# Kernel optimization log

Measured on AMD Instinct MI355X. Metric: run time of the kernel, lower is better.

## Reference

```python
import jax, jax.numpy as jnp
import numpy as np

B, SQ, SK, E, H = 2, 256, 512, 512, 256

def _lin_init(k, fan_in, fan_out):
    return jax.random.normal(k, (fan_in, fan_out), jnp.float32) / np.sqrt(fan_in)

def setup_inputs() -> dict:
    key = jax.random.key(0)
    ks = jax.random.split(key, 16)
    inp = {
        'query': jax.random.normal(ks[0], (B, SQ, E), jnp.float32),
        'key':   jax.random.normal(ks[1], (B, SK, E), jnp.float32),
        # encoders
        'Wqe': _lin_init(ks[2], E, H), 'bqe': jnp.zeros((H,), jnp.float32),
        'Wke': _lin_init(ks[3], E, H), 'bke': jnp.zeros((H,), jnp.float32),
        # importance predictor: Linear(2H,H) x1, Linear(H,H) x2, Linear(H,1)
        'W0': _lin_init(ks[4], 2 * H, H), 'b0': jnp.zeros((H,), jnp.float32),
        'W1': _lin_init(ks[5], H, H),     'b1': jnp.zeros((H,), jnp.float32),
        'W2': _lin_init(ks[6], H, H),     'b2': jnp.zeros((H,), jnp.float32),
        'Wf': _lin_init(ks[7], H, 1),     'bf': jnp.zeros((1,), jnp.float32),
        # variance estimator: Linear(2H,H), Linear(H,1), Softplus
        'Wv1': _lin_init(ks[8], 2 * H, H), 'bv1': jnp.zeros((H,), jnp.float32),
        'Wv2': _lin_init(ks[9], H, 1),     'bv2': jnp.zeros((1,), jnp.float32),
    }
    return inp

def reference(query, key, Wqe, bqe, Wke, bke, W0, b0, W1, b1, W2, b2, Wf, bf, Wv1, bv1, Wv2, bv2):
    # Encoders (dropout is identity at eval): [B,Sq,H] and [B,Sk,H]
    qf = jax.nn.relu(jnp.einsum('bqe,eh->bqh', query, Wqe) + bqe)
    kf = jax.nn.relu(jnp.einsum('bke,eh->bkh', key, Wke) + bke)

    # concat([qf, kf]) @ W == qf @ W[:H] + kf @ W[H:]; avoid materializing the 2H concat
    Hd = qf.shape[-1]
    # importance predictor, layer 0 over all (q,k) pairs -> [B,Sq,Sk,H]
    q_part = jnp.einsum('bqh,hd->bqd', qf, W0[:Hd])
    k_part = jnp.einsum('bkh,hd->bkd', kf, W0[Hd:])
    h = jax.nn.relu(q_part[:, :, None, :] + k_part[:, None, :, :] + b0)
    h = jax.nn.relu(jnp.einsum('bqkh,hd->bqkd', h, W1) + b1)
    h = jax.nn.relu(jnp.einsum('bqkh,hd->bqkd', h, W2) + b2)
    importance_logits = (jnp.einsum('bqkh,ho->bqko', h, Wf) + bf)[..., 0]  # [B,Sq,Sk]

    # variance estimator
    qv = jnp.einsum('bqh,hd->bqd', qf, Wv1[:Hd])
    kv = jnp.einsum('bkh,hd->bkd', kf, Wv1[Hd:])
    v = jax.nn.relu(qv[:, :, None, :] + kv[:, None, :, :] + bv1)
    variance = jax.nn.softplus((jnp.einsum('bqkh,ho->bqko', v, Wv2) + bv2)[..., 0])

    return importance_logits, variance
```

## Files before the change

### kernel.cpp

```cpp
#include <hip/hip_runtime.h>
#include <hip/hip_bf16.h>
#include <math.h>

typedef __attribute__((ext_vector_type(4))) float f32x4;
typedef __attribute__((ext_vector_type(8))) short short8;
typedef __attribute__((ext_vector_type(4))) short short4v;

#define H_DIM 256
#define SQ_DIM 256
#define SK_DIM 512
#define E_DIM 512
#define B_DIM 2

__global__ __launch_bounds__(256) void gemm_enc(const float* __restrict__ query,
                                                const float* __restrict__ key,
                                                const float* __restrict__ Wqe,
                                                const float* __restrict__ bqe,
                                                const float* __restrict__ Wke,
                                                const float* __restrict__ bke,
                                                float* __restrict__ qfkf)
{
    __shared__ float As[16][68];
    __shared__ float Bs[16][68];
    const int t  = threadIdx.x;
    const int m0 = blockIdx.y * 64, n0 = blockIdx.x * 64;
    const float* A;
    const float* B;
    const float* bias;
    if (m0 < 512) { A = query + (size_t)m0 * E_DIM; B = Wqe; bias = bqe; }
    else          { A = key + (size_t)(m0 - 512) * E_DIM; B = Wke; bias = bke; }

    const int tx = t & 15, ty = t >> 4;
    const int am = t >> 2, ak = (t & 3) * 4;
    const int bk = t >> 4, bn = (t & 15) * 4;

    float acc[4][4] = {};
    for (int k0 = 0; k0 < E_DIM; k0 += 16) {
        f32x4 av = *(const f32x4*)(A + (size_t)am * E_DIM + k0 + ak);
        f32x4 bv = *(const f32x4*)(B + (size_t)(k0 + bk) * H_DIM + n0 + bn);
        __syncthreads();
        As[ak + 0][am] = av[0];
        As[ak + 1][am] = av[1];
        As[ak + 2][am] = av[2];
        As[ak + 3][am] = av[3];
        *(f32x4*)&Bs[bk][bn] = bv;
        __syncthreads();
        #pragma unroll
        for (int kk = 0; kk < 16; ++kk) {
            f32x4 a  = *(const f32x4*)&As[kk][ty * 4];
            f32x4 bb = *(const f32x4*)&Bs[kk][tx * 4];
            #pragma unroll
            for (int i = 0; i < 4; ++i)
                #pragma unroll
                for (int j = 0; j < 4; ++j)
                    acc[i][j] += a[i] * bb[j];
        }
    }
    #pragma unroll
    for (int i = 0; i < 4; ++i) {
        f32x4 ov;
        #pragma unroll
        for (int j = 0; j < 4; ++j)
            ov[j] = fmaxf(acc[i][j] + bias[n0 + tx * 4 + j], 0.f);
        *(f32x4*)(qfkf + (size_t)(m0 + ty * 4 + i) * H_DIM + n0 + tx * 4) = ov;
    }
}

__global__ __launch_bounds__(256) void gemm_proj(const float* __restrict__ qfkf,
                                                 const float* __restrict__ W0,
                                                 const float* __restrict__ Wv1,
                                                 float* __restrict__ qpkp,
                                                 float* __restrict__ qvkv)
{
    __shared__ float As[16][68];
    __shared__ float Bs[16][68];
    const int t  = threadIdx.x;
    const int m0 = blockIdx.y * 64, n0 = blockIdx.x * 64;
    const int roff = (m0 < 512) ? 0 : 256;
    const float* A = qfkf + (size_t)m0 * H_DIM;
    const float* B = ((n0 < 256) ? W0 : Wv1) + (size_t)roff * H_DIM + (n0 & 255);
    float* C = ((n0 < 256) ? qpkp : qvkv) + (size_t)m0 * H_DIM + (n0 & 255);

    const int tx = t & 15, ty = t >> 4;
    const int am = t >> 2, ak = (t & 3) * 4;
    const int bk = t >> 4, bn = (t & 15) * 4;

    float acc[4][4] = {};
    for (int k0 = 0; k0 < H_DIM; k0 += 16) {
        f32x4 av = *(const f32x4*)(A + (size_t)am * H_DIM + k0 + ak);
        f32x4 bv = *(const f32x4*)(B + (size_t)(k0 + bk) * H_DIM + bn);
        __syncthreads();
        As[ak + 0][am] = av[0];
        As[ak + 1][am] = av[1];
        As[ak + 2][am] = av[2];
        As[ak + 3][am] = av[3];
        *(f32x4*)&Bs[bk][bn] = bv;
        __syncthreads();
        #pragma unroll
        for (int kk = 0; kk < 16; ++kk) {
            f32x4 a  = *(const f32x4*)&As[kk][ty * 4];
            f32x4 bb = *(const f32x4*)&Bs[kk][tx * 4];
            #pragma unroll
            for (int i = 0; i < 4; ++i)
                #pragma unroll
                for (int j = 0; j < 4; ++j)
                    acc[i][j] += a[i] * bb[j];
        }
    }
    #pragma unroll
    for (int i = 0; i < 4; ++i) {
        f32x4 ov;
        #pragma unroll
        for (int j = 0; j < 4; ++j) ov[j] = acc[i][j];
        *(f32x4*)(C + (size_t)(ty * 4 + i) * H_DIM + tx * 4) = ov;
    }
}

__global__ __launch_bounds__(256) void transpose_cast(const float* __restrict__ W1,
                                                      const float* __restrict__ W2,
                                                      __hip_bfloat16* __restrict__ T1,
                                                      __hip_bfloat16* __restrict__ T2)
{
    __shared__ float tile[64][65];
    const float* W = blockIdx.y ? W2 : W1;
    __hip_bfloat16* T = blockIdx.y ? T2 : T1;
    const int bx = blockIdx.x & 3, by = blockIdx.x >> 2;
    const int k0 = by * 64, n0 = bx * 64;
    const int t = threadIdx.x;
    #pragma unroll
    for (int i = 0; i < 16; ++i) {
        int r = (t >> 6) + i * 4;
        int c = t & 63;
        tile[r][c] = W[(size_t)(k0 + r) * 256 + n0 + c];
    }
    __syncthreads();
    #pragma unroll
    for (int i = 0; i < 16; ++i) {
        int r = (t >> 6) + i * 4;
        int c = t & 63;
        T[(size_t)(n0 + r) * 256 + k0 + c] = __float2bfloat16(tile[c][r]);
    }
}

__global__ __launch_bounds__(512, 2) void pair_main(
    const float* __restrict__ qp, const float* __restrict__ kp,
    const float* __restrict__ qv, const float* __restrict__ kv,
    const __hip_bfloat16* __restrict__ W1T, const __hip_bfloat16* __restrict__ W2T,
    const float* __restrict__ b0, const float* __restrict__ b1,
    const float* __restrict__ b2, const float* __restrict__ Wf,
    const float* __restrict__ bf_, const float* __restrict__ bv1,
    const float* __restrict__ Wv2, const float* __restrict__ bv2,
    float* __restrict__ out)
{
    extern __shared__ char smem[];
    char* hbuf  = smem;
    char* wbufA = smem + 65536;
    char* wbufB = smem + 81920;

    const int t    = threadIdx.x;
    const int lane = t & 63, wave = t >> 6;
    const int wm   = wave >> 2, wn = wave & 3;
    const int idx  = blockIdx.x;
    const int b    = idx >> 10;
    const int q    = (idx >> 2) & 255;
    const int kt   = idx & 3;
    const int k0g  = kt * 128;

    const float* qprow  = qp + (size_t)(b * SQ_DIM + q) * H_DIM;
    const float* kprows = kp + (size_t)(b * SK_DIM + k0g) * H_DIM;

    auto stage = [&](int g) {
        const __hip_bfloat16* Wsrc = (g < 8) ? W1T : W2T;
        char* wb = (g & 1) ? wbufB : wbufA;
        const int k0 = (g & 7) * 32;
        #pragma unroll
        for (int i = 0; i < 2; ++i) {
            int u = wave * 64 + i * 512 + lane;
            int n = u >> 2;
            int s_log = (u & 3) ^ ((n >> 1) & 3);
            const __hip_bfloat16* gp = Wsrc + n * H_DIM + k0 + s_log * 8;
            char* lp = wb + (wave * 64 + i * 512) * 16;
            __builtin_amdgcn_global_load_lds((const void*)gp, (void*)lp, 16, 0, 0);
        }
    };

    stage(0);

    #pragma unroll
    for (int i = 0; i < 8; ++i) {
        int cidx = t + 512 * i;
        int row  = cidx >> 5;
        int c8   = cidx & 31;
        const float* kr = kprows + row * H_DIM + c8 * 8;
        f32x4 k0v = *(const f32x4*)(kr);
        f32x4 k1v = *(const f32x4*)(kr + 4);
        f32x4 q0v = *(const f32x4*)(qprow + c8 * 8);
        f32x4 q1v = *(const f32x4*)(qprow + c8 * 8 + 4);
        f32x4 z0  = *(const f32x4*)(b0 + c8 * 8);
        f32x4 z1  = *(const f32x4*)(b0 + c8 * 8 + 4);
        short8 pk;
        #pragma unroll
        for (int j = 0; j < 4; ++j) {
            float v = fmaxf(k0v[j] + q0v[j] + z0[j], 0.f);
            float w = fmaxf(k1v[j] + q1v[j] + z1[j], 0.f);
            __hip_bfloat16 hv = __float2bfloat16(v);
            __hip_bfloat16 hw = __float2bfloat16(w);
            pk[j]     = __builtin_bit_cast(short, hv);
            pk[j + 4] = __builtin_bit_cast(short, hw);
        }
        int addr = (row * 512 + c8 * 16) ^ ((row & 7) << 4);
        *(short8*)(hbuf + addr) = pk;
    }
    __syncthreads();

    f32x4 acc[4][4];
    #pragma unroll
    for (int i = 0; i < 4; ++i)
        #pragma unroll
        for (int j = 0; j < 4; ++j)
            acc[i][j] = 0.f;

    auto gemm_step = [&](int c) {
        const char* wb = (c & 1) ? wbufB : wbufA;
        short8 bfrag[4];
        #pragma unroll
        for (int mt = 0; mt < 4; ++mt) {
            int m = 64 * wm + 16 * mt + (lane & 15);
            int addr = (m * 512 + c * 64 + ((lane >> 4) * 16)) ^ ((m & 7) << 4);
            bfrag[mt] = *(const short8*)(hbuf + addr);
        }
        #pragma unroll
        for (int nt = 0; nt < 4; ++nt) {
            int n = 64 * wn + 16 * nt + (lane & 15);
            int s_lds = (lane >> 4) ^ ((n >> 1) & 3);
            short8 afrag = *(const short8*)(wb + n * 64 + s_lds * 16);
            #pragma unroll
            for (int mt = 0; mt < 4; ++mt)
                acc[mt][nt] = __builtin_amdgcn_mfma_f32_16x16x32_bf16(afrag, bfrag[mt], acc[mt][nt], 0, 0, 0);
        }
    };

    for (int c = 0; c < 8; ++c) {
        stage(c + 1);
        gemm_step(c);
        __syncthreads();
    }

    #pragma unroll
    for (int mt = 0; mt < 4; ++mt) {
        int m = 64 * wm + 16 * mt + (lane & 15);
        #pragma unroll
        for (int nt = 0; nt < 4; ++nt) {
            int n0_ = 64 * wn + 16 * nt + ((lane >> 4) << 2);
            f32x4 bias = *(const f32x4*)(b1 + n0_);
            short4v pk;
            #pragma unroll
            for (int j = 0; j < 4; ++j) {
                float v = fmaxf(acc[mt][nt][j] + bias[j], 0.f);
                __hip_bfloat16 hv = __float2bfloat16(v);
                pk[j] = __builtin_bit_cast(short, hv);
            }
            int addr = (m * 512 + n0_ * 2) ^ ((m & 7) << 4);
            *(short4v*)(hbuf + addr) = pk;
            acc[mt][nt] = 0.f;
        }
    }
    __syncthreads();

    for (int c = 0; c < 8; ++c) {
        if (c < 7) stage(9 + c);
        gemm_step(c);
        __syncthreads();
    }

    float p[4];
    #pragma unroll
    for (int mt = 0; mt < 4; ++mt) {
        float s = 0.f;
        #pragma unroll
        for (int nt = 0; nt < 4; ++nt) {
            int n0_ = 64 * wn + 16 * nt + ((lane >> 4) << 2);
            f32x4 wf   = *(const f32x4*)(Wf + n0_);
            f32x4 bias = *(const f32x4*)(b2 + n0_);
            #pragma unroll
            for (int j = 0; j < 4; ++j)
                s += fmaxf(acc[mt][nt][j] + bias[j], 0.f) * wf[j];
        }
        s += __shfl_xor(s, 16);
        s += __shfl_xor(s, 32);
        p[mt] = s;
    }

    float* lpart = (float*)smem;
    if (lane < 16) {
        #pragma unroll
        for (int mt = 0; mt < 4; ++mt)
            lpart[(wm * 64 + mt * 16 + lane) * 4 + wn] = p[mt];
    }
    __syncthreads();

    const size_t obase = (size_t)(b * SQ_DIM + q) * SK_DIM + k0g;
    if (t < 128) {
        f32x4 v = *(const f32x4*)(lpart + t * 4);
        out[obase + t] = v[0] + v[1] + v[2] + v[3] + bf_[0];
    }

    {
        int r = t >> 2, s4 = t & 3;
        const float* qvrow = qv + (size_t)(b * SQ_DIM + q) * H_DIM;
        const float* kvrow = kv + (size_t)(b * SK_DIM + k0g + r) * H_DIM;
        float a = 0.f;
        #pragma unroll
        for (int i = 0; i < 16; ++i) {
            int cidx = s4 * 64 + i * 4;
            f32x4 x  = *(const f32x4*)(qvrow + cidx);
            f32x4 y  = *(const f32x4*)(kvrow + cidx);
            f32x4 bb = *(const f32x4*)(bv1 + cidx);
            f32x4 wv = *(const f32x4*)(Wv2 + cidx);
            #pragma unroll
            for (int j = 0; j < 4; ++j)
                a += fmaxf(x[j] + y[j] + bb[j], 0.f) * wv[j];
        }
        a += __shfl_xor(a, 1);
        a += __shfl_xor(a, 2);
        if (s4 == 0) {
            float xx = a + bv2[0];
            float sp = (xx > 20.f) ? xx : log1pf(expf(xx));
            out[(size_t)B_DIM * SQ_DIM * SK_DIM + obase + r] = sp;
        }
    }
}

extern "C" void kernel_launch(void* const* d_in, const int* in_sizes, int n_in,
                              void* d_out, int out_size, void* d_ws, size_t ws_size,
                              hipStream_t stream)
{
    (void)in_sizes; (void)n_in; (void)out_size; (void)ws_size;

    const float* query = (const float*)d_in[0];
    const float* key   = (const float*)d_in[1];
    const float* Wqe   = (const float*)d_in[2];
    const float* bqe   = (const float*)d_in[3];
    const float* Wke   = (const float*)d_in[4];
    const float* bke   = (const float*)d_in[5];
    const float* W0    = (const float*)d_in[6];
    const float* b0    = (const float*)d_in[7];
    const float* W1    = (const float*)d_in[8];
    const float* b1    = (const float*)d_in[9];
    const float* W2    = (const float*)d_in[10];
    const float* b2    = (const float*)d_in[11];
    const float* Wf    = (const float*)d_in[12];
    const float* bf    = (const float*)d_in[13];
    const float* Wv1   = (const float*)d_in[14];
    const float* bv1   = (const float*)d_in[15];
    const float* Wv2   = (const float*)d_in[16];
    const float* bv2   = (const float*)d_in[17];
    float* out = (float*)d_out;

    char* ws = (char*)d_ws;
    float* qfkf = (float*)(ws);
    float* qpkp = (float*)(ws + 1572864);
    float* qvkv = (float*)(ws + 3145728);
    __hip_bfloat16* W1T = (__hip_bfloat16*)(ws + 4718592);
    __hip_bfloat16* W2T = (__hip_bfloat16*)(ws + 4849664);

    const float* qp = qpkp;
    const float* kp = qpkp + 512 * 256;
    const float* qv = qvkv;
    const float* kv = qvkv + 512 * 256;

    (void)hipFuncSetAttribute((const void*)pair_main,
                              hipFuncAttributeMaxDynamicSharedMemorySize, 98304);

    transpose_cast<<<dim3(16, 2), 256, 0, stream>>>(W1, W2, W1T, W2T);
    gemm_enc<<<dim3(4, 24), 256, 0, stream>>>(query, key, Wqe, bqe, Wke, bke, qfkf);
    gemm_proj<<<dim3(8, 24), 256, 0, stream>>>(qfkf, W0, Wv1, qpkp, qvkv);
    pair_main<<<dim3(2048), 512, 98304, stream>>>(qp, kp, qv, kv, W1T, W2T,
                                                  b0, b1, b2, Wf, bf, bv1, Wv2, bv2, out);
}
```

Measured before the change: 333.4 us.

## Use split-bf16 MFMA for encoder/projection GEMMs and single-buffer pair kernel

Replaces the two FP32 SIMT GEMMs (encoder and projection) with MFMA bf16 GEMMs. Each FP32 operand is split into a high and a low bf16 part and three MFMA products are summed, which keeps accuracy close to FP32. Pair_main drops from a double-buffered weight stage to a single buffer, cutting LDS from 96KB to 80KB and raising launch bounds to 4 blocks. It also reorders the block index mapping so blocks sharing the same q across batches are adjacent. In exchange it adds extra cast/transpose kernels and an extra barrier per chunk in pair_main.

```diff
diff --git a/kernel.cpp b/kernel.cpp
--- a/kernel.cpp
+++ b/kernel.cpp
@@ -12,107 +12,67 @@
 #define E_DIM 512
 #define B_DIM 2
 
-__global__ __launch_bounds__(256) void gemm_enc(const float* __restrict__ query,
-                                                const float* __restrict__ key,
-                                                const float* __restrict__ Wqe,
-                                                const float* __restrict__ bqe,
-                                                const float* __restrict__ Wke,
-                                                const float* __restrict__ bke,
-                                                float* __restrict__ qfkf)
-{
-    __shared__ float As[16][68];
-    __shared__ float Bs[16][68];
-    const int t  = threadIdx.x;
-    const int m0 = blockIdx.y * 64, n0 = blockIdx.x * 64;
-    const float* A;
-    const float* B;
-    const float* bias;
-    if (m0 < 512) { A = query + (size_t)m0 * E_DIM; B = Wqe; bias = bqe; }
-    else          { A = key + (size_t)(m0 - 512) * E_DIM; B = Wke; bias = bke; }
-
-    const int tx = t & 15, ty = t >> 4;
-    const int am = t >> 2, ak = (t & 3) * 4;
-    const int bk = t >> 4, bn = (t & 15) * 4;
-
-    float acc[4][4] = {};
-    for (int k0 = 0; k0 < E_DIM; k0 += 16) {
-        f32x4 av = *(const f32x4*)(A + (size_t)am * E_DIM + k0 + ak);
-        f32x4 bv = *(const f32x4*)(B + (size_t)(k0 + bk) * H_DIM + n0 + bn);
-        __syncthreads();
-        As[ak + 0][am] = av[0];
-        As[ak + 1][am] = av[1];
-        As[ak + 2][am] = av[2];
-        As[ak + 3][am] = av[3];
-        *(f32x4*)&Bs[bk][bn] = bv;
-        __syncthreads();
-        #pragma unroll
-        for (int kk = 0; kk < 16; ++kk) {
-            f32x4 a  = *(const f32x4*)&As[kk][ty * 4];
-            f32x4 bb = *(const f32x4*)&Bs[kk][tx * 4];
-            #pragma unroll
-            for (int i = 0; i < 4; ++i)
-                #pragma unroll
-                for (int j = 0; j < 4; ++j)
-                    acc[i][j] += a[i] * bb[j];
-        }
-    }
-    #pragma unroll
-    for (int i = 0; i < 4; ++i) {
-        f32x4 ov;
-        #pragma unroll
-        for (int j = 0; j < 4; ++j)
-            ov[j] = fmaxf(acc[i][j] + bias[n0 + tx * 4 + j], 0.f);
-        *(f32x4*)(qfkf + (size_t)(m0 + ty * 4 + i) * H_DIM + n0 + tx * 4) = ov;
-    }
-}
-
-__global__ __launch_bounds__(256) void gemm_proj(const float* __restrict__ qfkf,
-                                                 const float* __restrict__ W0,
-                                                 const float* __restrict__ Wv1,
-                                                 float* __restrict__ qpkp,
-                                                 float* __restrict__ qvkv)
-{
-    __shared__ float As[16][68];
-    __shared__ float Bs[16][68];
-    const int t  = threadIdx.x;
-    const int m0 = blockIdx.y * 64, n0 = blockIdx.x * 64;
-    const int roff = (m0 < 512) ? 0 : 256;
-    const float* A = qfkf + (size_t)m0 * H_DIM;
-    const float* B = ((n0 < 256) ? W0 : Wv1) + (size_t)roff * H_DIM + (n0 & 255);
-    float* C = ((n0 < 256) ? qpkp : qvkv) + (size_t)m0 * H_DIM + (n0 & 255);
-
-    const int tx = t & 15, ty = t >> 4;
-    const int am = t >> 2, ak = (t & 3) * 4;
-    const int bk = t >> 4, bn = (t & 15) * 4;
-
-    float acc[4][4] = {};
-    for (int k0 = 0; k0 < H_DIM; k0 += 16) {
-        f32x4 av = *(const f32x4*)(A + (size_t)am * H_DIM + k0 + ak);
-        f32x4 bv = *(const f32x4*)(B + (size_t)(k0 + bk) * H_DIM + bn);
-        __syncthreads();
-        As[ak + 0][am] = av[0];
-        As[ak + 1][am] = av[1];
-        As[ak + 2][am] = av[2];
-        As[ak + 3][am] = av[3];
-        *(f32x4*)&Bs[bk][bn] = bv;
-        __syncthreads();
-        #pragma unroll
-        for (int kk = 0; kk < 16; ++kk) {
-            f32x4 a  = *(const f32x4*)&As[kk][ty * 4];
-            f32x4 bb = *(const f32x4*)&Bs[kk][tx * 4];
-            #pragma unroll
-            for (int i = 0; i < 4; ++i)
-                #pragma unroll
-                for (int j = 0; j < 4; ++j)
-                    acc[i][j] += a[i] * bb[j];
-        }
-    }
-    #pragma unroll
-    for (int i = 0; i < 4; ++i) {
-        f32x4 ov;
-        #pragma unroll
-        for (int j = 0; j < 4; ++j) ov[j] = acc[i][j];
-        *(f32x4*)(C + (size_t)(ty * 4 + i) * H_DIM + tx * 4) = ov;
+__global__ __launch_bounds__(256) void split_cast(const float* __restrict__ query,
+                                                  const float* __restrict__ key,
+                                                  __hip_bfloat16* __restrict__ A1)
+{
+    int gid = blockIdx.x * 256 + threadIdx.x;
+    int m  = gid >> 7;
+    int kq = gid & 127;
+    const float* src = (m < 512) ? query + (size_t)m * 512
+                                 : key + (size_t)(m - 512) * 512;
+    f32x4 v = *(const f32x4*)(src + kq * 4);
+    short4v hv, lv;
+    #pragma unroll
+    for (int j = 0; j < 4; ++j) {
+        __hip_bfloat16 h = __float2bfloat16(v[j]);
+        float lf = v[j] - __bfloat162float(h);
+        __hip_bfloat16 l = __float2bfloat16(lf);
+        hv[j] = __builtin_bit_cast(short, h);
+        lv[j] = __builtin_bit_cast(short, l);
+    }
+    *(short4v*)(A1 + (size_t)m * 1024 + kq * 4) = hv;
+    *(short4v*)(A1 + (size_t)m * 1024 + 512 + kq * 4) = lv;
+}
+
+__global__ __launch_bounds__(256) void transpose_split(
+    const float* __restrict__ Wqe, const float* __restrict__ Wke,
+    const float* __restrict__ W0,  const float* __restrict__ Wv1,
+    __hip_bfloat16* __restrict__ Benc, __hip_bfloat16* __restrict__ Bproj)
+{
+    __shared__ float tile[64][65];
+    const float* S = nullptr; __hip_bfloat16* D = nullptr; int KJ = 256;
+    switch (blockIdx.y) {
+        case 0: S = Wqe;             D = Benc;                       KJ = 512; break;
+        case 1: S = Wke;             D = Benc + 256 * 1024;          KJ = 512; break;
+        case 2: S = W0;              D = Bproj;                      KJ = 256; break;
+        case 3: S = Wv1;             D = Bproj + 256 * 512;          KJ = 256; break;
+        case 4: S = W0 + 256 * 256;  D = Bproj + 512 * 512;          KJ = 256; break;
+        case 5: S = Wv1 + 256 * 256; D = Bproj + 512 * 512 + 256 * 512; KJ = 256; break;
+    }
+    const int dstStride = 2 * KJ;
+    const int ntile = 4 * (KJ >> 6);
+    const int x = blockIdx.x;
+    if (x >= ntile) return;
+    const int tx = x & 3, ty = x >> 2;
+    const int k0 = ty * 64, n0 = tx * 64;
+    const int t = threadIdx.x;
+    #pragma unroll
+    for (int i = 0; i < 16; ++i) {
+        int r = (t >> 6) + i * 4;
+        int c = t & 63;
+        tile[r][c] = S[(size_t)(k0 + r) * 256 + n0 + c];
+    }
+    __syncthreads();
+    #pragma unroll
+    for (int i = 0; i < 16; ++i) {
+        int r = (t >> 6) + i * 4;
+        int c = t & 63;
+        float v = tile[c][r];
+        __hip_bfloat16 h = __float2bfloat16(v);
+        float lf = v - __bfloat162float(h);
+        D[(size_t)(n0 + r) * dstStride + k0 + c] = h;
+        D[(size_t)(n0 + r) * dstStride + KJ + k0 + c] = __float2bfloat16(lf);
     }
 }
 
@@ -142,7 +102,106 @@
     }
 }
 
-__global__ __launch_bounds__(512, 2) void pair_main(
+template<int KD, bool SPLIT_OUT>
+__global__ __launch_bounds__(256) void gemm3(
+    const __hip_bfloat16* __restrict__ Apl,
+    const __hip_bfloat16* __restrict__ B0,
+    const __hip_bfloat16* __restrict__ B1,
+    const float* __restrict__ bias0, const float* __restrict__ bias1,
+    __hip_bfloat16* __restrict__ outS,
+    float* __restrict__ outF0, float* __restrict__ outF1)
+{
+    __shared__ char smem[32768];
+    const int t = threadIdx.x, lane = t & 63, wave = t >> 6;
+    const int wm = wave >> 1, wn = wave & 1;
+    const int m0 = blockIdx.y * 64, n0 = blockIdx.x * 64;
+    const __hip_bfloat16* Arow = Apl + (size_t)m0 * (2 * KD);
+    const __hip_bfloat16* Brow = ((m0 < 512) ? B0 : B1) + (size_t)n0 * (2 * KD);
+
+    auto stage = [&](int c) {
+        char* wb = smem + ((c & 1) << 14);
+        const int k0 = c * 32;
+        #pragma unroll
+        for (int i = 0; i < 4; ++i) {
+            int u = wave * 64 + lane + i * 256;
+            int r = u >> 2;
+            int sl = (u & 3) ^ ((r >> 1) & 3);
+            int isB = r >> 7;
+            int rr = r & 127;
+            const __hip_bfloat16* base = isB ? Brow : Arow;
+            const __hip_bfloat16* gp = base + (size_t)(rr >> 1) * (2 * KD)
+                                       + (rr & 1) * KD + k0 + sl * 8;
+            char* lp = wb + (wave * 64 + i * 256) * 16;
+            __builtin_amdgcn_global_load_lds((const void*)gp, (void*)lp, 16, 0, 0);
+        }
+    };
+
+    stage(0);
+    __syncthreads();
+    f32x4 acc[2][2];
+    #pragma unroll
+    for (int i = 0; i < 2; ++i)
+        #pragma unroll
+        for (int j = 0; j < 2; ++j) acc[i][j] = 0.f;
+
+    const int NCH = KD / 32;
+    for (int c = 0; c < NCH; ++c) {
+        if (c + 1 < NCH) stage(c + 1);
+        const char* wb = smem + ((c & 1) << 14);
+        short8 ah[2], al[2];
+        #pragma unroll
+        for (int nt = 0; nt < 2; ++nt) {
+            int n = wn * 32 + nt * 16 + (lane & 15);
+            int rh = 128 + 2 * n, rl = rh + 1;
+            ah[nt] = *(const short8*)(wb + rh * 64 + (((lane >> 4) ^ ((rh >> 1) & 3)) << 4));
+            al[nt] = *(const short8*)(wb + rl * 64 + (((lane >> 4) ^ ((rl >> 1) & 3)) << 4));
+        }
+        #pragma unroll
+        for (int mt = 0; mt < 2; ++mt) {
+            int m = wm * 32 + mt * 16 + (lane & 15);
+            int rh = 2 * m, rl = rh + 1;
+            short8 bh = *(const short8*)(wb + rh * 64 + (((lane >> 4) ^ ((rh >> 1) & 3)) << 4));
+            short8 bl = *(const short8*)(wb + rl * 64 + (((lane >> 4) ^ ((rl >> 1) & 3)) << 4));
+            #pragma unroll
+            for (int nt = 0; nt < 2; ++nt) {
+                acc[mt][nt] = __builtin_amdgcn_mfma_f32_16x16x32_bf16(ah[nt], bh, acc[mt][nt], 0, 0, 0);
+                acc[mt][nt] = __builtin_amdgcn_mfma_f32_16x16x32_bf16(al[nt], bh, acc[mt][nt], 0, 0, 0);
+                acc[mt][nt] = __builtin_amdgcn_mfma_f32_16x16x32_bf16(ah[nt], bl, acc[mt][nt], 0, 0, 0);
+            }
+        }
+        __syncthreads();
+    }
+
+    #pragma unroll
+    for (int mt = 0; mt < 2; ++mt) {
+        int m = m0 + wm * 32 + mt * 16 + (lane & 15);
+        #pragma unroll
+        for (int nt = 0; nt < 2; ++nt) {
+            int nb = n0 + wn * 32 + nt * 16 + ((lane >> 4) << 2);
+            if (SPLIT_OUT) {
+                const float* bias = (m0 < 512) ? bias0 : bias1;
+                f32x4 bv = *(const f32x4*)(bias + nb);
+                short4v hv, lv;
+                #pragma unroll
+                for (int j = 0; j < 4; ++j) {
+                    float v = fmaxf(acc[mt][nt][j] + bv[j], 0.f);
+                    __hip_bfloat16 h = __float2bfloat16(v);
+                    float lf = v - __bfloat162float(h);
+                    hv[j] = __builtin_bit_cast(short, h);
+                    lv[j] = __builtin_bit_cast(short, __float2bfloat16(lf));
+                }
+                *(short4v*)(outS + (size_t)m * 512 + nb) = hv;
+                *(short4v*)(outS + (size_t)m * 512 + 256 + nb) = lv;
+            } else {
+                float* o = (nb < 256) ? outF0 + (size_t)m * 256 + nb
+                                      : outF1 + (size_t)m * 256 + (nb - 256);
+                *(f32x4*)o = acc[mt][nt];
+            }
+        }
+    }
+}
+
+__global__ __launch_bounds__(512, 4) void pair_main(
     const float* __restrict__ qp, const float* __restrict__ kp,
     const float* __restrict__ qv, const float* __restrict__ kv,
     const __hip_bfloat16* __restrict__ W1T, const __hip_bfloat16* __restrict__ W2T,
@@ -153,17 +212,16 @@
     float* __restrict__ out)
 {
     extern __shared__ char smem[];
-    char* hbuf  = smem;
-    char* wbufA = smem + 65536;
-    char* wbufB = smem + 81920;
+    char* hbuf = smem;
+    char* wbuf = smem + 65536;
 
     const int t    = threadIdx.x;
     const int lane = t & 63, wave = t >> 6;
     const int wm   = wave >> 2, wn = wave & 3;
     const int idx  = blockIdx.x;
-    const int b    = idx >> 10;
-    const int q    = (idx >> 2) & 255;
+    const int q    = idx >> 3;
     const int kt   = idx & 3;
+    const int b    = (idx >> 2) & 1;
     const int k0g  = kt * 128;
 
     const float* qprow  = qp + (size_t)(b * SQ_DIM + q) * H_DIM;
@@ -171,7 +229,6 @@
 
     auto stage = [&](int g) {
         const __hip_bfloat16* Wsrc = (g < 8) ? W1T : W2T;
-        char* wb = (g & 1) ? wbufB : wbufA;
         const int k0 = (g & 7) * 32;
         #pragma unroll
         for (int i = 0; i < 2; ++i) {
@@ -179,7 +236,7 @@
             int n = u >> 2;
             int s_log = (u & 3) ^ ((n >> 1) & 3);
             const __hip_bfloat16* gp = Wsrc + n * H_DIM + k0 + s_log * 8;
-            char* lp = wb + (wave * 64 + i * 512) * 16;
+            char* lp = wbuf + (wave * 64 + i * 512) * 16;
             __builtin_amdgcn_global_load_lds((const void*)gp, (void*)lp, 16, 0, 0);
         }
     };
@@ -220,31 +277,30 @@
         for (int j = 0; j < 4; ++j)
             acc[i][j] = 0.f;
 
-    auto gemm_step = [&](int c) {
-        const char* wb = (c & 1) ? wbufB : wbufA;
-        short8 bfrag[4];
+    auto chunk = [&](int c, int g_next, bool do_stage) {
+        short8 afrag[4];
+        #pragma unroll
+        for (int nt = 0; nt < 4; ++nt) {
+            int n = 64 * wn + 16 * nt + (lane & 15);
+            int s_lds = (lane >> 4) ^ ((n >> 1) & 3);
+            afrag[nt] = *(const short8*)(wbuf + n * 64 + s_lds * 16);
+        }
+        __syncthreads();
+        if (do_stage) stage(g_next);
         #pragma unroll
         for (int mt = 0; mt < 4; ++mt) {
             int m = 64 * wm + 16 * mt + (lane & 15);
             int addr = (m * 512 + c * 64 + ((lane >> 4) * 16)) ^ ((m & 7) << 4);
-            bfrag[mt] = *(const short8*)(hbuf + addr);
-        }
-        #pragma unroll
-        for (int nt = 0; nt < 4; ++nt) {
-            int n = 64 * wn + 16 * nt + (lane & 15);
-            int s_lds = (lane >> 4) ^ ((n >> 1) & 3);
-            short8 afrag = *(const short8*)(wb + n * 64 + s_lds * 16);
+            short8 bfrag = *(const short8*)(hbuf + addr);
             #pragma unroll
-            for (int mt = 0; mt < 4; ++mt)
-                acc[mt][nt] = __builtin_amdgcn_mfma_f32_16x16x32_bf16(afrag, bfrag[mt], acc[mt][nt], 0, 0, 0);
-        }
+            for (int nt = 0; nt < 4; ++nt)
+                acc[mt][nt] = __builtin_amdgcn_mfma_f32_16x16x32_bf16(afrag[nt], bfrag, acc[mt][nt], 0, 0, 0);
+        }
+        __syncthreads();
     };
 
-    for (int c = 0; c < 8; ++c) {
-        stage(c + 1);
-        gemm_step(c);
-        __syncthreads();
-    }
+    for (int c = 0; c < 8; ++c)
+        chunk(c, c + 1, true);
 
     #pragma unroll
     for (int mt = 0; mt < 4; ++mt) {
@@ -267,11 +323,8 @@
     }
     __syncthreads();
 
-    for (int c = 0; c < 8; ++c) {
-        if (c < 7) stage(9 + c);
-        gemm_step(c);
-        __syncthreads();
-    }
+    for (int c = 0; c < 8; ++c)
+        chunk(c, 9 + c, c < 7);
 
     float p[4];
     #pragma unroll
@@ -358,11 +411,14 @@
     float* out = (float*)d_out;
 
     char* ws = (char*)d_ws;
-    float* qfkf = (float*)(ws);
-    float* qpkp = (float*)(ws + 1572864);
-    float* qvkv = (float*)(ws + 3145728);
-    __hip_bfloat16* W1T = (__hip_bfloat16*)(ws + 4718592);
-    __hip_bfloat16* W2T = (__hip_bfloat16*)(ws + 4849664);
+    __hip_bfloat16* A1    = (__hip_bfloat16*)(ws);
+    __hip_bfloat16* Aq    = (__hip_bfloat16*)(ws + 3145728);
+    __hip_bfloat16* Benc  = (__hip_bfloat16*)(ws + 4718592);
+    __hip_bfloat16* Bproj = (__hip_bfloat16*)(ws + 5767168);
+    __hip_bfloat16* W1T   = (__hip_bfloat16*)(ws + 6815744);
+    __hip_bfloat16* W2T   = (__hip_bfloat16*)(ws + 6946816);
+    float* qpkp = (float*)(ws);
+    float* qvkv = (float*)(ws + 1572864);
 
     const float* qp = qpkp;
     const float* kp = qpkp + 512 * 256;
@@ -370,11 +426,15 @@
     const float* kv = qvkv + 512 * 256;
 
     (void)hipFuncSetAttribute((const void*)pair_main,
-                              hipFuncAttributeMaxDynamicSharedMemorySize, 98304);
+                              hipFuncAttributeMaxDynamicSharedMemorySize, 81920);
 
     transpose_cast<<<dim3(16, 2), 256, 0, stream>>>(W1, W2, W1T, W2T);
-    gemm_enc<<<dim3(4, 24), 256, 0, stream>>>(query, key, Wqe, bqe, Wke, bke, qfkf);
-    gemm_proj<<<dim3(8, 24), 256, 0, stream>>>(qfkf, W0, Wv1, qpkp, qvkv);
-    pair_main<<<dim3(2048), 512, 98304, stream>>>(qp, kp, qv, kv, W1T, W2T,
+    split_cast<<<dim3(768), 256, 0, stream>>>(query, key, A1);
+    transpose_split<<<dim3(32, 6), 256, 0, stream>>>(Wqe, Wke, W0, Wv1, Benc, Bproj);
+    gemm3<512, true><<<dim3(4, 24), 256, 0, stream>>>(
+        A1, Benc, Benc + 256 * 1024, bqe, bke, Aq, nullptr, nullptr);
+    gemm3<256, false><<<dim3(8, 24), 256, 0, stream>>>(
+        Aq, Bproj, Bproj + 512 * 512, nullptr, nullptr, nullptr, qpkp, qvkv);
+    pair_main<<<dim3(2048), 512, 81920, stream>>>(qp, kp, qv, kv, W1T, W2T,
                                                   b0, b1, b2, Wf, bf, bv1, Wv2, bv2, out);
 }
```

Result: faster. 326.8 us (-2.0%).
